# Kernel optimization log

Measured on AMD Instinct MI355X. Metric: run time of the kernel, lower is better.

## Reference

```python
import jax, jax.numpy as jnp
import numpy as np

N_NODES = 50_000
N_EDGES = 1_600_000
D = 128          # input_dim == hidden_dim
L = 3            # num_layers
NUM_GRAPHS = 64
LN_EPS = 1e-5


def setup_inputs() -> dict:
    key = jax.random.key(0)
    ks = jax.random.split(key, 12)
    x = jax.random.normal(ks[0], (N_NODES, D), dtype=jnp.float32)
    edge_index = jax.random.randint(ks[1], (2, N_EDGES), 0, N_NODES, dtype=jnp.int64)
    edge_weight = jax.random.normal(ks[2], (N_EDGES,), dtype=jnp.float32)  # signed
    batch = jnp.sort(jax.random.randint(ks[3], (N_NODES,), 0, NUM_GRAPHS, dtype=jnp.int64))
    W_pos = jax.random.normal(ks[4], (L, D, D), dtype=jnp.float32) * 0.05
    b_pos = jnp.zeros((L, D), dtype=jnp.float32)
    W_neg = jax.random.normal(ks[5], (L, D, D), dtype=jnp.float32) * 0.05
    b_neg = jnp.zeros((L, D), dtype=jnp.float32)
    ln_gamma = jnp.ones((D,), dtype=jnp.float32)
    ln_beta = jnp.zeros((D,), dtype=jnp.float32)
    return dict(x=x, edge_index=edge_index, edge_weight=edge_weight, batch=batch,
                W_pos=W_pos, b_pos=b_pos, W_neg=W_neg, b_neg=b_neg,
                ln_gamma=ln_gamma, ln_beta=ln_beta)


def gcn_conv(x, src, dst, w, W, b):
    """PyG GCNConv with edge weights: lin -> sym-normalized scatter-add -> +bias.
    Self-loops (weight 1) are handled analytically instead of appending edges.
    Edges with weight 0 contribute nothing (equivalent to sign-masking the edge set)."""
    n = x.shape[0]
    xw = x @ W                                              # [N, D]
    deg = jax.ops.segment_sum(w, dst, num_segments=n) + 1.0  # +1 for self-loop; >= 1
    dinv = jax.lax.rsqrt(deg)                                # deg^{-1/2}
    norm = dinv[src] * w * dinv[dst]                         # [E]
    agg = jax.ops.segment_sum(norm[:, None] * xw[src], dst, num_segments=n)
    agg = agg + (dinv * dinv)[:, None] * xw                  # self-loop message: xw / deg
    return agg + b


def reference(x, edge_index, edge_weight, batch, W_pos, b_pos, W_neg, b_neg, ln_gamma, ln_beta):
    src, dst = edge_index[0], edge_index[1]
    # sign-split as zero-weight edges: identical math to boolean-masked edge subsets
    w_pos = jnp.maximum(edge_weight, 0.0)
    w_neg = jnp.maximum(-edge_weight, 0.0)
    for l in range(L):
        px = gcn_conv(x, src, dst, w_pos, W_pos[l], b_pos[l])
        nx = gcn_conv(x, src, dst, w_neg, W_neg[l], b_neg[l])
        x = jax.nn.relu(px) - jax.nn.relu(nx)
    # global_mean_pool
    sums = jax.ops.segment_sum(x, batch, num_segments=NUM_GRAPHS)
    counts = jax.ops.segment_sum(jnp.ones((x.shape[0],), x.dtype), batch, num_segments=NUM_GRAPHS)
    pooled = sums / jnp.maximum(counts, 1.0)[:, None]        # [G, D]
    # LayerNorm over feature dim
    mu = pooled.mean(-1, keepdims=True)
    var = ((pooled - mu) ** 2).mean(-1, keepdims=True)
    return (pooled - mu) * jax.lax.rsqrt(var + LN_EPS) * ln_gamma + ln_beta
```

## Files before the change

kernel.cpp:

```cpp
#include <hip/hip_runtime.h>
#include <hip/hip_fp16.h>

#define D 128
#define NG 64
#define WPB 4
#define TILE 4096
#define BSH 7
#define BNODES 128
#define CAP 4608
#define MASK40 ((1ULL << 40) - 1)
#define FPSCALE 1048576.0f
#define INV_FPSCALE (1.0f / 1048576.0f)
typedef unsigned int uint;
typedef unsigned long long u64;
typedef _Float16 f16x8 __attribute__((ext_vector_type(8)));
typedef float f32x4 __attribute__((ext_vector_type(4)));

__global__ void k_prep(const float* __restrict__ x, __half* __restrict__ xo,
                       const float* __restrict__ Wp, const float* __restrict__ Wn,
                       __half* __restrict__ wpt, __half* __restrict__ wnt,
                       float* sums, float* cnt, int* bktcur,
                       int total2, int nbuk) {
    int i = blockIdx.x * blockDim.x + threadIdx.x;
    if (i < total2) {
        float2 f = ((const float2*)x)[i];
        ((__half2*)xo)[i] = __floats2half2_rn(f.x, f.y);
    }
    if (i < 3 * 128 * 128) {
        int l = i >> 14;
        int r = i & 16383;
        int col = r >> 7, k = r & 127;
        size_t src = ((size_t)l << 14) + ((size_t)k << 7) + col;
        wpt[i] = __float2half_rn(Wp[src]);
        wnt[i] = __float2half_rn(Wn[src]);
    }
    if (i < NG * D) sums[i] = 0.0f;
    if (i < NG) cnt[i] = 0.0f;
    if (i < nbuk) bktcur[i] = i * CAP;
}

__global__ __launch_bounds__(256) void k_bucket(const int* __restrict__ ei,
                                                const float* __restrict__ ew,
                                                int* bktcur, uint2* rec,
                                                int E, int nbuk) {
    __shared__ int h[512];
    __shared__ int cur[512];
    int t = threadIdx.x;
    for (int b = t; b < 512; b += 256) h[b] = 0;
    __syncthreads();
    int lo = blockIdx.x * TILE, hi = min(E, lo + TILE);
    for (int e = lo + t; e < hi; e += 256)
        atomicAdd(&h[ei[(size_t)E + e] >> BSH], 1);
    __syncthreads();
    for (int b = t; b < nbuk; b += 256)
        if (h[b]) cur[b] = atomicAdd(&bktcur[b], h[b]);
    __syncthreads();
    for (int e = lo + t; e < hi; e += 256) {
        int dst = ei[(size_t)E + e];
        int src = ei[e];
        float w = ew[e];
        int bkt = dst >> BSH;
        int pos = atomicAdd(&cur[bkt], 1);
        if (pos < (bkt + 1) * CAP)
            rec[pos] = make_uint2((uint)src | ((uint)(dst & (BNODES - 1)) << 16),
                                  __float_as_uint(w));
    }
}

__global__ __launch_bounds__(256) void k_deg(const uint2* __restrict__ rec,
                                             const int* __restrict__ bktcur,
                                             float2* dpn, int* row_ptr,
                                             int* cend, int* cpos, int n) {
    __shared__ u64 accp[BNODES], accn[BNODES];
    __shared__ int s[BNODES];
    int b = blockIdx.x, t = threadIdx.x;
    if (t < BNODES) { accp[t] = 0ULL; accn[t] = 0ULL; }
    __syncthreads();
    int lo = b * CAP, hi = bktcur[b];
    for (int i = lo + t; i < hi; i += 256) {
        uint2 r = rec[i];
        int dl = (r.x >> 16) & (BNODES - 1);
        float w = __uint_as_float(r.y);
        u64 pkt = (1ULL << 40) | (u64)(fabsf(w) * FPSCALE + 0.5f);
        atomicAdd((w < 0.0f) ? &accn[dl] : &accp[dl], pkt);
    }
    __syncthreads();
    int cp = 0, cn = 0, cnt_t = 0;
    u64 p = 0, q = 0;
    if (t < BNODES) {
        p = accp[t]; q = accn[t];
        cp = (int)(p >> 40); cn = (int)(q >> 40);
        cnt_t = cp + cn;
        s[t] = cnt_t;
    }
    __syncthreads();
    for (int off = 1; off < BNODES; off <<= 1) {
        int u = 0;
        if (t < BNODES && t >= off) u = s[t - off];
        __syncthreads();
        if (t < BNODES) s[t] += u;
        __syncthreads();
    }
    if (t < BNODES) {
        int node = b * BNODES + t;
        if (node < n) {
            int base = b * CAP + s[t] - cnt_t;
            row_ptr[node] = base;
            cend[node] = base + cnt_t;
            cpos[node] = cp;
            float2 dd;
            dd.x = rsqrtf(1.0f + (float)(p & MASK40) * INV_FPSCALE);
            dd.y = rsqrtf(1.0f + (float)(q & MASK40) * INV_FPSCALE);
            dpn[node] = dd;
        }
    }
}

__global__ __launch_bounds__(256) void k_csr(const uint2* __restrict__ rec,
                                             const int* __restrict__ bktcur,
                                             const int* __restrict__ row_ptr,
                                             const int* __restrict__ cpos,
                                             const float2* __restrict__ dpn,
                                             uint* pack, int n) {
    __shared__ int curp[BNODES], curn[BNODES];
    int b = blockIdx.x, t = threadIdx.x;
    if (t < BNODES) {
        int node = b * BNODES + t;
        if (node < n) {
            int rp = row_ptr[node];
            curp[t] = rp;
            curn[t] = rp + cpos[node];
        } else { curp[t] = 0; curn[t] = 0; }
    }
    __syncthreads();
    int lo = b * CAP, hi = bktcur[b];
    for (int i = lo + t; i < hi; i += 256) {
        uint2 r = rec[i];
        int src = r.x & 0xFFFFu;
        int dl = (r.x >> 16) & (BNODES - 1);
        float w = __uint_as_float(r.y);
        float2 dd = dpn[src];
        float v;
        int slot;
        if (w < 0.0f) { v = dd.y * (-w); slot = atomicAdd(&curn[dl], 1); }
        else          { v = dd.x * w;    slot = atomicAdd(&curp[dl], 1); }
        pack[slot] = (uint)src | ((uint)__half_as_ushort(__float2half_rn(v)) << 16);
    }
}

__global__ __launch_bounds__(64 * WPB) void k_gather(
    const __half* __restrict__ x16, const uint* __restrict__ pack,
    const int* __restrict__ row_ptr, const int* __restrict__ cend,
    const int* __restrict__ cpos, const float2* __restrict__ dpn,
    __half* __restrict__ tp, __half* __restrict__ tn, int n) {
    __shared__ uint eb[WPB][136];
    const int w = threadIdx.x >> 6;
    const int lane = threadIdx.x & 63;
    const int q = lane >> 4;
    const int c = lane & 15;
    const int node = blockIdx.x * WPB + w;
    if (node >= n) return;
    const int beg = row_ptr[node], end = cend[node];
    const int mid = beg + cpos[node];
    const float2 dd = dpn[node];
    const uint4* __restrict__ x4u = (const uint4*)x16;
    uint* ebw = eb[w];

    uint4 xv = x4u[(size_t)node * 16 + c];
    float xf[8];
    {
        float2 f;
        f = __half22float2(*(__half2*)&xv.x); xf[0] = f.x; xf[1] = f.y;
        f = __half22float2(*(__half2*)&xv.y); xf[2] = f.x; xf[3] = f.y;
        f = __half22float2(*(__half2*)&xv.z); xf[4] = f.x; xf[5] = f.y;
        f = __half22float2(*(__half2*)&xv.w); xf[6] = f.x; xf[7] = f.y;
    }

#pragma unroll
    for (int part = 0; part < 2; ++part) {
        const int lo = part ? mid : beg;
        const int hi = part ? end : mid;
        const float ds = part ? dd.y : dd.x;
        float a0[8], a1[8];
        const float s0 = (q == 0) ? ds : 0.0f;
#pragma unroll
        for (int j = 0; j < 8; ++j) { a0[j] = s0 * xf[j]; a1[j] = 0.0f; }
        for (int cb = lo; cb < hi; cb += 128) {
            int m = hi - cb;
            if (m > 128) m = 128;
            const int mp = (m + 7) & ~7;
            for (int i = lane; i < mp; i += 64)
                ebw[i] = (i < m) ? pack[cb + i] : 0u;
            for (int i = 0; i < mp; i += 8) {
                const uint pk0 = ebw[i + q];
                const uint pk1 = ebw[i + 4 + q];
                const uint4 y0 = x4u[(size_t)(pk0 & 0xFFFFu) * 16 + c];
                const uint4 y1 = x4u[(size_t)(pk1 & 0xFFFFu) * 16 + c];
                const float v0 =
                    __half2float(__ushort_as_half((unsigned short)(pk0 >> 16)));
                const float v1 =
                    __half2float(__ushort_as_half((unsigned short)(pk1 >> 16)));
                float2 f;
                f = __half22float2(*(__half2*)&y0.x);
                a0[0] = fmaf(v0, f.x, a0[0]); a0[1] = fmaf(v0, f.y, a0[1]);
                f = __half22float2(*(__half2*)&y0.y);
                a0[2] = fmaf(v0, f.x, a0[2]); a0[3] = fmaf(v0, f.y, a0[3]);
                f = __half22float2(*(__half2*)&y0.z);
                a0[4] = fmaf(v0, f.x, a0[4]); a0[5] = fmaf(v0, f.y, a0[5]);
                f = __half22float2(*(__half2*)&y0.w);
                a0[6] = fmaf(v0, f.x, a0[6]); a0[7] = fmaf(v0, f.y, a0[7]);
                f = __half22float2(*(__half2*)&y1.x);
                a1[0] = fmaf(v1, f.x, a1[0]); a1[1] = fmaf(v1, f.y, a1[1]);
                f = __half22float2(*(__half2*)&y1.y);
                a1[2] = fmaf(v1, f.x, a1[2]); a1[3] = fmaf(v1, f.y, a1[3]);
                f = __half22float2(*(__half2*)&y1.z);
                a1[4] = fmaf(v1, f.x, a1[4]); a1[5] = fmaf(v1, f.y, a1[5]);
                f = __half22float2(*(__half2*)&y1.w);
                a1[6] = fmaf(v1, f.x, a1[6]); a1[7] = fmaf(v1, f.y, a1[7]);
            }
        }
#pragma unroll
        for (int j = 0; j < 8; ++j) {
            a0[j] += a1[j];
            a0[j] += __shfl_down(a0[j], 32);
            a0[j] += __shfl_down(a0[j], 16);
        }
        if (q == 0) {
            __half2 h0 = __floats2half2_rn(ds * a0[0], ds * a0[1]);
            __half2 h1 = __floats2half2_rn(ds * a0[2], ds * a0[3]);
            __half2 h2 = __floats2half2_rn(ds * a0[4], ds * a0[5]);
            __half2 h3 = __floats2half2_rn(ds * a0[6], ds * a0[7]);
            uint4 st;
            st.x = *(uint*)&h0; st.y = *(uint*)&h1;
            st.z = *(uint*)&h2; st.w = *(uint*)&h3;
            ((uint4*)(part ? tn : tp))[(size_t)node * 16 + c] = st;
        }
    }
}

__global__ __launch_bounds__(256) void k_gemm(
    const __half* __restrict__ tp, const __half* __restrict__ tn,
    const __half* __restrict__ wpt, const __half* __restrict__ wnt,
    const float* __restrict__ bp, const float* __restrict__ bn,
    __half* __restrict__ xout, int nrows) {
    __shared__ __half wlds[2][128][136];
    const int tid = threadIdx.x;
    {
        const uint4* wp4 = (const uint4*)wpt;
        const uint4* wn4 = (const uint4*)wnt;
#pragma unroll
        for (int j = 0; j < 8; ++j) {
            int idx = tid + j * 256;
            int col = idx >> 4;
            int k8 = idx & 15;
            *(uint4*)&wlds[0][col][k8 * 8] = wp4[idx];
            *(uint4*)&wlds[1][col][k8 * 8] = wn4[idx];
        }
    }
    const int wave = tid >> 6;
    const int lane = tid & 63;
    const int cl = lane & 15;
    const int quad = lane >> 4;
    const int row_blk = blockIdx.x * 64 + wave * 16;
    __syncthreads();
    if (row_blk >= nrows) return;
    int arow = row_blk + cl;
    if (arow >= nrows) arow = nrows - 1;
    const f16x8* __restrict__ tpr = (const f16x8*)(tp + (size_t)arow * 128);
    const f16x8* __restrict__ tnr = (const f16x8*)(tn + (size_t)arow * 128);
    f16x8 ap[4], an[4];
#pragma unroll
    for (int kb = 0; kb < 4; ++kb) {
        ap[kb] = tpr[kb * 4 + quad];
        an[kb] = tnr[kb * 4 + quad];
    }
#pragma unroll
    for (int ct = 0; ct < 8; ++ct) {
        const int col = ct * 16 + cl;
        f32x4 accp = {0.0f, 0.0f, 0.0f, 0.0f};
        f32x4 accn = {0.0f, 0.0f, 0.0f, 0.0f};
#pragma unroll
        for (int kb = 0; kb < 4; ++kb) {
            f16x8 wfp = *(const f16x8*)&wlds[0][col][kb * 32 + quad * 8];
            f16x8 wfn = *(const f16x8*)&wlds[1][col][kb * 32 + quad * 8];
            accp = __builtin_amdgcn_mfma_f32_16x16x32_f16(ap[kb], wfp, accp, 0, 0, 0);
            accn = __builtin_amdgcn_mfma_f32_16x16x32_f16(an[kb], wfn, accn, 0, 0, 0);
        }
        const float bpv = bp[col], bnv = bn[col];
#pragma unroll
        for (int reg = 0; reg < 4; ++reg) {
            int row = row_blk + quad * 4 + reg;
            if (row < nrows) {
                float pv = accp[reg] + bpv;
                float nv = accn[reg] + bnv;
                xout[(size_t)row * 128 + col] =
                    __float2half_rn(fmaxf(pv, 0.0f) - fmaxf(nv, 0.0f));
            }
        }
    }
}

__global__ __launch_bounds__(128) void k_pool(
    const __half* __restrict__ x, const int* __restrict__ batch,
    float* sums, float* cnt, int n) {
    int f = threadIdx.x;
    int n0 = blockIdx.x * 64;
    int n1 = min(n0 + 64, n);
    float acc = 0.0f;
    int g_prev = batch[n0];
    int local = 0;
    for (int i = n0; i < n1; ++i) {
        int g = batch[i];
        if (g != g_prev) {
            atomicAdd(&sums[g_prev * D + f], acc);
            if (f == 0) atomicAdd(&cnt[g_prev], (float)local);
            acc = 0.0f; local = 0; g_prev = g;
        }
        acc += __half2float(x[(size_t)i * D + f]);
        local++;
    }
    atomicAdd(&sums[g_prev * D + f], acc);
    if (f == 0) atomicAdd(&cnt[g_prev], (float)local);
}

__global__ __launch_bounds__(128) void k_ln(
    const float* __restrict__ sums, const float* __restrict__ cnt,
    const float* __restrict__ gamma, const float* __restrict__ beta,
    float* __restrict__ out) {
    __shared__ float red[128];
    int g = blockIdx.x, f = threadIdx.x;
    float c = fmaxf(cnt[g], 1.0f);
    float v = sums[g * D + f] / c;
    red[f] = v;
    __syncthreads();
    for (int off = 64; off > 0; off >>= 1) {
        if (f < off) red[f] += red[f + off];
        __syncthreads();
    }
    float mu = red[0] / (float)D;
    __syncthreads();
    float d = v - mu;
    red[f] = d * d;
    __syncthreads();
    for (int off = 64; off > 0; off >>= 1) {
        if (f < off) red[f] += red[f + off];
        __syncthreads();
    }
    float var = red[0] / (float)D;
    out[g * D + f] = d * rsqrtf(var + 1e-5f) * gamma[f] + beta[f];
}

extern "C" void kernel_launch(void* const* d_in, const int* in_sizes, int n_in,
                              void* d_out, int out_size, void* d_ws,
                              size_t ws_size, hipStream_t stream) {
    const float* x     = (const float*)d_in[0];
    const int*   ei    = (const int*)d_in[1];
    const float* ew    = (const float*)d_in[2];
    const int*   bat   = (const int*)d_in[3];
    const float* Wp    = (const float*)d_in[4];
    const float* bp    = (const float*)d_in[5];
    const float* Wn    = (const float*)d_in[6];
    const float* bn    = (const float*)d_in[7];
    const float* gamma = (const float*)d_in[8];
    const float* beta  = (const float*)d_in[9];
    const int n = in_sizes[0] / D;
    const int E = in_sizes[2];
    const int NBUK = (n + BNODES - 1) >> BSH;
    const int NBLK = (E + TILE - 1) / TILE;

    float* ws = (float*)d_ws;
    size_t off = 0;
    auto alloc = [&](size_t elems) {
        float* p = ws + off;
        off += (elems + 63) & ~(size_t)63;
        return p;
    };
    __half* x16  = (__half*)alloc((size_t)n * D / 2);
    __half* tpb  = (__half*)alloc((size_t)n * D / 2);
    __half* tnb  = (__half*)alloc((size_t)n * D / 2);
    __half* xb   = (__half*)alloc((size_t)n * D / 2);
    __half* wpt  = (__half*)alloc(3 * 128 * 128 / 2);
    __half* wnt  = (__half*)alloc(3 * 128 * 128 / 2);
    float2* dpn  = (float2*)alloc((size_t)2 * n);
    float* sums  = alloc(NG * D);
    float* cnt   = alloc(NG);
    int* bktcur  = (int*)alloc(NBUK);
    int* row_ptr = (int*)alloc(n);
    int* cend    = (int*)alloc(n);
    int* cpos    = (int*)alloc(n);
    uint2* rec   = (uint2*)alloc((size_t)NBUK * CAP * 2);
    uint* pack   = (uint*)alloc((size_t)NBUK * CAP);

    k_prep<<<(n * D / 2 + 255) / 256, 256, 0, stream>>>(
        x, x16, Wp, Wn, wpt, wnt, sums, cnt, bktcur, n * D / 2, NBUK);
    k_bucket<<<NBLK, 256, 0, stream>>>(ei, ew, bktcur, rec, E, NBUK);
    k_deg<<<NBUK, 256, 0, stream>>>(rec, bktcur, dpn, row_ptr, cend, cpos, n);
    k_csr<<<NBUK, 256, 0, stream>>>(rec, bktcur, row_ptr, cpos, dpn, pack, n);

    const __half* xcur = x16;
    for (int l = 0; l < 3; ++l) {
        k_gather<<<(n + WPB - 1) / WPB, 64 * WPB, 0, stream>>>(
            xcur, pack, row_ptr, cend, cpos, dpn, tpb, tnb, n);
        k_gemm<<<(n + 63) / 64, 256, 0, stream>>>(
            tpb, tnb, wpt + (size_t)l * 128 * 128, wnt + (size_t)l * 128 * 128,
            bp + (size_t)l * D, bn + (size_t)l * D, xb, n);
        xcur = xb;
    }
    k_pool<<<(n + 63) / 64, 128, 0, stream>>>(xb, bat, sums, cnt, n);
    k_ln<<<NG, 128, 0, stream>>>(sums, cnt, gamma, beta, (float*)d_out);
}
```

Measured before the change: 395.4 us.

## Stage bucketed edge records in LDS for grouped global writes; vectorize x conversion

```diff
diff --git a/kernel.cpp b/kernel.cpp
--- a/kernel.cpp
+++ b/kernel.cpp
@@ -20,11 +20,15 @@
                        const float* __restrict__ Wp, const float* __restrict__ Wn,
                        __half* __restrict__ wpt, __half* __restrict__ wnt,
                        float* sums, float* cnt, int* bktcur,
-                       int total2, int nbuk) {
+                       int total4, int nbuk) {
     int i = blockIdx.x * blockDim.x + threadIdx.x;
-    if (i < total2) {
-        float2 f = ((const float2*)x)[i];
-        ((__half2*)xo)[i] = __floats2half2_rn(f.x, f.y);
+    if (i < total4) {
+        float4 f = ((const float4*)x)[i];
+        __half2 h0 = __floats2half2_rn(f.x, f.y);
+        __half2 h1 = __floats2half2_rn(f.z, f.w);
+        uint2 st;
+        st.x = *(uint*)&h0; st.y = *(uint*)&h1;
+        ((uint2*)xo)[i] = st;
     }
     if (i < 3 * 128 * 128) {
         int l = i >> 14;
@@ -43,27 +47,53 @@
                                                 const float* __restrict__ ew,
                                                 int* bktcur, uint2* rec,
                                                 int E, int nbuk) {
-    __shared__ int h[512];
-    __shared__ int cur[512];
+    __shared__ int h2[256];
+    __shared__ int lofs[512];
+    __shared__ int gbase[512];
+    __shared__ int lcur[512];
+    __shared__ uint2 stg[TILE];
     int t = threadIdx.x;
-    for (int b = t; b < 512; b += 256) h[b] = 0;
+    lofs[t] = 0; lofs[t + 256] = 0;
     __syncthreads();
     int lo = blockIdx.x * TILE, hi = min(E, lo + TILE);
+    int m = hi - lo;
     for (int e = lo + t; e < hi; e += 256)
-        atomicAdd(&h[ei[(size_t)E + e] >> BSH], 1);
-    __syncthreads();
-    for (int b = t; b < nbuk; b += 256)
-        if (h[b]) cur[b] = atomicAdd(&bktcur[b], h[b]);
+        atomicAdd(&lofs[ei[(size_t)E + e] >> BSH], 1);
+    __syncthreads();
+    int c0 = lofs[2 * t], c1 = lofs[2 * t + 1];
+    if (c0) gbase[2 * t] = atomicAdd(&bktcur[2 * t], c0);
+    if (c1) gbase[2 * t + 1] = atomicAdd(&bktcur[2 * t + 1], c1);
+    h2[t] = c0 + c1;
+    __syncthreads();
+    for (int off = 1; off < 256; off <<= 1) {
+        int u = (t >= off) ? h2[t - off] : 0;
+        __syncthreads();
+        h2[t] += u;
+        __syncthreads();
+    }
+    int excl = h2[t] - (c0 + c1);
+    lofs[2 * t] = excl;
+    lofs[2 * t + 1] = excl + c0;
+    lcur[2 * t] = excl;
+    lcur[2 * t + 1] = excl + c0;
     __syncthreads();
     for (int e = lo + t; e < hi; e += 256) {
         int dst = ei[(size_t)E + e];
         int src = ei[e];
         float w = ew[e];
-        int bkt = dst >> BSH;
-        int pos = atomicAdd(&cur[bkt], 1);
-        if (pos < (bkt + 1) * CAP)
-            rec[pos] = make_uint2((uint)src | ((uint)(dst & (BNODES - 1)) << 16),
-                                  __float_as_uint(w));
+        int b = dst >> BSH;
+        int pos = atomicAdd(&lcur[b], 1);
+        stg[pos] = make_uint2((uint)src | ((uint)(dst & (BNODES - 1)) << 16) |
+                                  ((uint)b << 23),
+                              __float_as_uint(w));
+    }
+    __syncthreads();
+    for (int i = t; i < m; i += 256) {
+        uint2 r = stg[i];
+        int b = (int)(r.x >> 23);
+        int gpos = gbase[b] + (i - lofs[b]);
+        if (gpos < (b + 1) * CAP)
+            rec[gpos] = r;
     }
 }
 
@@ -391,8 +421,8 @@
     uint2* rec   = (uint2*)alloc((size_t)NBUK * CAP * 2);
     uint* pack   = (uint*)alloc((size_t)NBUK * CAP);
 
-    k_prep<<<(n * D / 2 + 255) / 256, 256, 0, stream>>>(
-        x, x16, Wp, Wn, wpt, wnt, sums, cnt, bktcur, n * D / 2, NBUK);
+    k_prep<<<(n * D / 4 + 255) / 256, 256, 0, stream>>>(
+        x, x16, Wp, Wn, wpt, wnt, sums, cnt, bktcur, n * D / 4, NBUK);
     k_bucket<<<NBLK, 256, 0, stream>>>(ei, ew, bktcur, rec, E, NBUK);
     k_deg<<<NBUK, 256, 0, stream>>>(rec, bktcur, dpn, row_ptr, cend, cpos, n);
     k_csr<<<NBUK, 256, 0, stream>>>(rec, bktcur, row_ptr, cpos, dpn, pack, n);
```

After: 393.5 us. About the same (-0.5%).
